# Optimization experiments

Hardware: AMD Instinct MI355X
Metric: run time of the kernel (lower is better)

The kernel has to match this reference:

```python
import jax, jax.numpy as jnp
import numpy as np

BATCH = 65536
INPUT_DIM = 128
NUM_KNOTS = 10
DEGREE = 3  # n_basis = NUM_KNOTS - DEGREE - 1 = 6


def bspline_basis(x, knots, degree):
    """Cox-de Boor B-spline basis, vectorized over all batch/feature entries.

    x: [B, D] (already clipped into [knots[0], knots[-1]))
    knots: [K] uniform knot vector
    returns: [B, D, K - degree - 1]
    """
    xe = x[..., None]                                            # [B, D, 1]
    # degree-0 indicator basis: [B, D, K-1]
    B = ((xe >= knots[:-1]) & (xe < knots[1:])).astype(x.dtype)
    for d in range(1, degree + 1):
        left_den = knots[d:-1] - knots[:-(d + 1)]                # [K-1-d]
        right_den = knots[d + 1:] - knots[1:-d]                  # [K-1-d]
        safe_l = jnp.where(left_den > 0, left_den, 1.0)
        safe_r = jnp.where(right_den > 0, right_den, 1.0)
        left = jnp.where(left_den > 0, (xe - knots[:-(d + 1)]) / safe_l, 0.0) * B[..., :-1]
        right = jnp.where(right_den > 0, (knots[d + 1:] - xe) / safe_r, 0.0) * B[..., 1:]
        B = left + right                                          # [B, D, K-1-d]
    return B


def setup_inputs() -> dict:
    key = jax.random.key(0)
    k1, k2 = jax.random.split(key)
    x = jax.random.normal(k1, (BATCH, INPUT_DIM), dtype=jnp.float32)
    interaction_weights = jax.random.normal(k2, (INPUT_DIM, INPUT_DIM), dtype=jnp.float32)
    return {"x": x, "interaction_weights": interaction_weights}


def reference(x, interaction_weights):
    # Shared uniform knot vector over [-1, 1], identical across all features
    knots = jnp.linspace(-1.0, 1.0, NUM_KNOTS).astype(x.dtype)
    eps = 1e-6
    xc = jnp.clip(x, knots[0], knots[-1] - eps)
    basis = bspline_basis(xc, knots, DEGREE)                     # [B, D, 6]
    B_sz = x.shape[0]
    basis_flat = basis.reshape(B_sz, -1)                         # [B, D*6]
    # interaction: out[b, j] = sum_i x[b,i]^2 * sigmoid(W[i,j])
    # (equivalent to bmm(x^T, x * sigmoid(W)) in the original, without
    #  materializing the [B, D, D] broadcast intermediate)
    S = jax.nn.sigmoid(interaction_weights)                      # [D, D]
    interaction = (x * x) @ S                                    # [B, D]
    return jnp.concatenate([basis_flat, interaction], axis=1)    # [B, D*6 + D]
```

## Files before the change

### kernel.cpp

```cpp
#include <hip/hip_runtime.h>
#include <math.h>

#define BATCH 65536
#define DIM 128
#define NBAS 6
#define OUTW 896
#define ROWS_PER_TILE 32
#define LDS_F4 33
#define LDS_F 132

typedef float f4v __attribute__((ext_vector_type(4)));

__global__ __launch_bounds__(256) void sigmoid_k(const float* __restrict__ W,
                                                 float* __restrict__ S) {
    int t = blockIdx.x * 256 + threadIdx.x;
    float w = W[t];
    S[t] = 1.0f / (1.0f + expf(-w));
}

__device__ __forceinline__ void bw(float x, int& s,
                                   float& w0, float& w1, float& w2, float& w3) {
    const float i6 = 0.16666666666666666f;
    float xc = fminf(fmaxf(x, -1.0f), 1.0f - 1e-6f);
    float p  = (xc + 1.0f) * 4.5f;
    float sf = floorf(p);
    float u  = p - sf;
    s = (int)sf;
    float u2 = u * u;
    float v  = 1.0f - u;
    w0 = u * u2 * i6;
    w1 = (((-3.0f * u + 3.0f) * u + 3.0f) * u + 1.0f) * i6;
    w2 = ((3.0f * u - 6.0f) * u2 + 4.0f) * i6;
    w3 = v * v * v * i6;
}

__device__ __forceinline__ float pick4(float w0, float w1, float w2, float w3, int d) {
    float r = 0.0f;
    r = (d == 0) ? w0 : r;
    r = (d == 1) ? w1 : r;
    r = (d == 2) ? w2 : r;
    r = (d == 3) ? w3 : r;
    return r;
}

__global__ __launch_bounds__(256, 8) void kan_main(const float* __restrict__ X,
                                                   const float* __restrict__ S,
                                                   float* __restrict__ out) {
    __shared__ __align__(16) float xTf[ROWS_PER_TILE * LDS_F];

    const int tid = threadIdx.x;
    const int row0 = blockIdx.x * ROWS_PER_TILE;

    const float4* X4 = (const float4*)(X + (size_t)row0 * DIM);
    float4* xT4 = (float4*)xTf;
#pragma unroll
    for (int k = 0; k < 4; ++k) {
        int e4 = k * 256 + tid;
        int r = e4 >> 5;
        int i4 = e4 & 31;
        xT4[r * LDS_F4 + i4] = X4[e4];
    }
    __syncthreads();

    {
        const int c = tid & 31;
        const int r0 = (tid >> 5) * 4;

        float acc[4][4];
#pragma unroll
        for (int rr = 0; rr < 4; ++rr)
#pragma unroll
            for (int q = 0; q < 4; ++q) acc[rr][q] = 0.0f;

        const float4* S4 = (const float4*)S;
        const float* xp0 = xTf + (r0 + 0) * LDS_F;
        const float* xp1 = xTf + (r0 + 1) * LDS_F;
        const float* xp2 = xTf + (r0 + 2) * LDS_F;
        const float* xp3 = xTf + (r0 + 3) * LDS_F;
#pragma unroll 2
        for (int i = 0; i < DIM; ++i) {
            float4 s = S4[i * 32 + c];
            float x0 = xp0[i], x1 = xp1[i], x2 = xp2[i], x3 = xp3[i];
            float xq[4] = {x0 * x0, x1 * x1, x2 * x2, x3 * x3};
#pragma unroll
            for (int rr = 0; rr < 4; ++rr) {
#pragma unroll
                for (int q = 0; q < 4; ++q) {
                    float sv = (q == 0) ? s.x : (q == 1) ? s.y : (q == 2) ? s.z : s.w;
                    acc[rr][q] = fmaf(xq[rr], sv, acc[rr][q]);
                }
            }
        }

#pragma unroll
        for (int rr = 0; rr < 4; ++rr) {
            f4v v = {acc[rr][0], acc[rr][1], acc[rr][2], acc[rr][3]};
            __builtin_nontemporal_store(
                v, (f4v*)(out + (size_t)(row0 + r0 + rr) * OUTW + DIM * NBAS + 4 * c));
        }
    }

    {
        const int lane = tid & 63;
        const int wv = tid >> 6;

        int fAh[3], fBh[3], tbh[3];
        bool uBh[3];
#pragma unroll
        for (int t = 0; t < 3; ++t) {
            int j = t * 64 + lane;
            int m = j % 3;
            int o0 = 4 * j;
            int fA = o0 / 6;
            fAh[t] = fA;
            fBh[t] = (fA < 127) ? fA + 1 : 127;
            tbh[t] = (m == 0) ? 0 : (m == 2) ? 2 : 4;
            uBh[t] = (m == 1);
        }

#pragma unroll 2
        for (int rr = 0; rr < 8; ++rr) {
            int r = rr * 4 + wv;
            const float* xrow = xTf + r * LDS_F;
            float* orow = out + (size_t)(row0 + r) * OUTW;
#pragma unroll
            for (int t = 0; t < 3; ++t) {
                float xA = xrow[fAh[t]];
                float xB = xrow[fBh[t]];
                int sA, sB;
                float a0, a1, a2, a3, b0, b1, b2, b3;
                bw(xA, sA, a0, a1, a2, a3);
                bw(xB, sB, b0, b1, b2, b3);
                int dA = sA - tbh[t];
                float r0v = pick4(a0, a1, a2, a3, dA);
                float r1v = pick4(a0, a1, a2, a3, dA - 1);
                float r2v = uBh[t] ? pick4(b0, b1, b2, b3, sB)
                                   : pick4(a0, a1, a2, a3, dA - 2);
                float r3v = uBh[t] ? pick4(b0, b1, b2, b3, sB - 1)
                                   : pick4(a0, a1, a2, a3, dA - 3);
                f4v v = {r0v, r1v, r2v, r3v};
                __builtin_nontemporal_store(v, (f4v*)(orow + 4 * (t * 64 + lane)));
            }
        }
    }
}

extern "C" void kernel_launch(void* const* d_in, const int* in_sizes, int n_in,
                              void* d_out, int out_size, void* d_ws, size_t ws_size,
                              hipStream_t stream) {
    const float* X = (const float*)d_in[0];
    const float* W = (const float*)d_in[1];
    float* out = (float*)d_out;
    float* S = (float*)d_ws;

    sigmoid_k<<<(DIM * DIM) / 256, 256, 0, stream>>>(W, S);
    kan_main<<<BATCH / ROWS_PER_TILE, 256, 0, stream>>>(X, S, out);
}
```

Before: 290.5 us.

## Stage B-spline basis in LDS via scatter, then stream out coalesced chunks

Each thread now evaluates the cubic basis once per feature and scatters the four nonzero weights into a zeroed LDS buffer holding 8 rows. The buffer is then written to global memory as coalesced float4 nontemporal stores and re-zeroed, looping over four chunks. This replaces the old scheme, where each output float4 recomputed up to two basis evaluations and chose values with selects. The cost is two extra barriers per chunk, roughly 24KB more LDS per block, and the occupancy hint drops from 8 to 4, which could hurt latency hiding. The x tile padding is also removed, which may add LDS bank conflicts in the matmul reads.

```diff
diff --git a/kernel.cpp b/kernel.cpp
--- a/kernel.cpp
+++ b/kernel.cpp
@@ -6,8 +6,10 @@
 #define NBAS 6
 #define OUTW 896
 #define ROWS_PER_TILE 32
-#define LDS_F4 33
-#define LDS_F 132
+#define CHROWS 8
+#define NCHUNK 4
+#define XT_F 128
+#define BAS_F 768
 
 typedef float f4v __attribute__((ext_vector_type(4)));
 
@@ -34,19 +36,11 @@
     w3 = v * v * v * i6;
 }
 
-__device__ __forceinline__ float pick4(float w0, float w1, float w2, float w3, int d) {
-    float r = 0.0f;
-    r = (d == 0) ? w0 : r;
-    r = (d == 1) ? w1 : r;
-    r = (d == 2) ? w2 : r;
-    r = (d == 3) ? w3 : r;
-    return r;
-}
-
-__global__ __launch_bounds__(256, 8) void kan_main(const float* __restrict__ X,
+__global__ __launch_bounds__(256, 4) void kan_main(const float* __restrict__ X,
                                                    const float* __restrict__ S,
                                                    float* __restrict__ out) {
-    __shared__ __align__(16) float xTf[ROWS_PER_TILE * LDS_F];
+    __shared__ __align__(16) float xTf[ROWS_PER_TILE * XT_F];
+    __shared__ __align__(16) float bas[CHROWS * BAS_F];
 
     const int tid = threadIdx.x;
     const int row0 = blockIdx.x * ROWS_PER_TILE;
@@ -56,10 +50,12 @@
 #pragma unroll
     for (int k = 0; k < 4; ++k) {
         int e4 = k * 256 + tid;
-        int r = e4 >> 5;
-        int i4 = e4 & 31;
-        xT4[r * LDS_F4 + i4] = X4[e4];
+        xT4[e4] = X4[e4];
     }
+    f4v z4 = {0.0f, 0.0f, 0.0f, 0.0f};
+    f4v* bas4 = (f4v*)bas;
+#pragma unroll
+    for (int k = 0; k < 6; ++k) bas4[k * 256 + tid] = z4;
     __syncthreads();
 
     {
@@ -73,10 +69,10 @@
             for (int q = 0; q < 4; ++q) acc[rr][q] = 0.0f;
 
         const float4* S4 = (const float4*)S;
-        const float* xp0 = xTf + (r0 + 0) * LDS_F;
-        const float* xp1 = xTf + (r0 + 1) * LDS_F;
-        const float* xp2 = xTf + (r0 + 2) * LDS_F;
-        const float* xp3 = xTf + (r0 + 3) * LDS_F;
+        const float* xp0 = xTf + (r0 + 0) * XT_F;
+        const float* xp1 = xTf + (r0 + 1) * XT_F;
+        const float* xp2 = xTf + (r0 + 2) * XT_F;
+        const float* xp3 = xTf + (r0 + 3) * XT_F;
 #pragma unroll 2
         for (int i = 0; i < DIM; ++i) {
             float4 s = S4[i * 32 + c];
@@ -101,46 +97,37 @@
     }
 
     {
-        const int lane = tid & 63;
-        const int wv = tid >> 6;
+        const int sr = tid >> 5;
+        const int f0 = tid & 31;
+        for (int c = 0; c < NCHUNK; ++c) {
+            const float* xrow = xTf + (c * CHROWS + sr) * XT_F;
+            float* basr = bas + sr * BAS_F;
+#pragma unroll
+            for (int m = 0; m < 4; ++m) {
+                int f = f0 + 32 * m;
+                float x = xrow[f];
+                int s;
+                float w0, w1, w2, w3;
+                bw(x, s, w0, w1, w2, w3);
+                float* bp = basr + f * NBAS + s;
+                if (s <= 5)           bp[0]  = w0;
+                if (s >= 1 && s <= 6) bp[-1] = w1;
+                if (s >= 2 && s <= 7) bp[-2] = w2;
+                if (s >= 3)           bp[-3] = w3;
+            }
+            __syncthreads();
 
-        int fAh[3], fBh[3], tbh[3];
-        bool uBh[3];
+            float* ob = out + (size_t)(row0 + c * CHROWS) * OUTW;
 #pragma unroll
-        for (int t = 0; t < 3; ++t) {
-            int j = t * 64 + lane;
-            int m = j % 3;
-            int o0 = 4 * j;
-            int fA = o0 / 6;
-            fAh[t] = fA;
-            fBh[t] = (fA < 127) ? fA + 1 : 127;
-            tbh[t] = (m == 0) ? 0 : (m == 2) ? 2 : 4;
-            uBh[t] = (m == 1);
-        }
-
-#pragma unroll 2
-        for (int rr = 0; rr < 8; ++rr) {
-            int r = rr * 4 + wv;
-            const float* xrow = xTf + r * LDS_F;
-            float* orow = out + (size_t)(row0 + r) * OUTW;
-#pragma unroll
-            for (int t = 0; t < 3; ++t) {
-                float xA = xrow[fAh[t]];
-                float xB = xrow[fBh[t]];
-                int sA, sB;
-                float a0, a1, a2, a3, b0, b1, b2, b3;
-                bw(xA, sA, a0, a1, a2, a3);
-                bw(xB, sB, b0, b1, b2, b3);
-                int dA = sA - tbh[t];
-                float r0v = pick4(a0, a1, a2, a3, dA);
-                float r1v = pick4(a0, a1, a2, a3, dA - 1);
-                float r2v = uBh[t] ? pick4(b0, b1, b2, b3, sB)
-                                   : pick4(a0, a1, a2, a3, dA - 2);
-                float r3v = uBh[t] ? pick4(b0, b1, b2, b3, sB - 1)
-                                   : pick4(a0, a1, a2, a3, dA - 3);
-                f4v v = {r0v, r1v, r2v, r3v};
-                __builtin_nontemporal_store(v, (f4v*)(orow + 4 * (t * 64 + lane)));
+            for (int k = 0; k < 6; ++k) {
+                int idx = k * 256 + tid;
+                int r = idx / 192;
+                int j = idx - r * 192;
+                f4v v = bas4[idx];
+                __builtin_nontemporal_store(v, (f4v*)(ob + (size_t)r * OUTW + 4 * j));
+                bas4[idx] = z4;
             }
+            __syncthreads();
         }
     }
 }
```

Result: faster. 284.5 us (-2.1%).
